# Kernel optimization log

Hardware: AMD Instinct MI355X
Metric: run time of the kernel (lower is better)

Reference implementation:

```python
import jax, jax.numpy as jnp
import numpy as np

TEMP = 0.3
EPS = 1e-09
EPS2 = 1e-10


def _unit(v):
    return v / jnp.linalg.norm(v, axis=-1, keepdims=True)


def setup_inputs() -> dict:
    key = jax.random.key(0)
    k1, k2 = jax.random.split(key)
    T, Q, D, K = 512, 8, 64, 16  # tracks, queries/track, embed dim, detections/track
    x = _unit(jax.random.normal(k1, (T * K, D), dtype=jnp.float32))
    y = _unit(jax.random.normal(k2, (T, Q, D), dtype=jnp.float32))
    track_idxs = jnp.repeat(jnp.arange(T, dtype=jnp.int64), K)  # every track id present
    return {"x": x, "track_idxs": track_idxs, "y": y}


def reference(x, track_idxs, y):
    # local_contrast=True, separate_tracks=False, static_contrast=False,
    # use_hard_condition=False, shift_to_positive=False (module defaults).
    T, Q, D = y.shape
    # All track ids 0..T-1 appear in track_idxs (by construction), so
    # ut_ids = unique(track_idxs) = arange(T) and y[ut_ids] = y.
    ut_ids = jnp.arange(T, dtype=track_idxs.dtype)
    y_flat = y.reshape(T * Q, D)          # flatten(0,1)
    y_idxs = jnp.tile(ut_ids, Q)          # ut_ids.repeat(Q) in torch semantics
    # Pairwise exp-scaled similarities: [N, T*Q]
    S = jnp.exp(jnp.einsum("nd,md->nm", x, y_flat) / TEMP)
    # Positive pairs: same track id (each x row belongs to exactly one uid),
    # so the per-uid loop collapses to one masked reduction.
    M = track_idxs[:, None] == y_idxs[None, :]
    num = jnp.sum(jnp.where(M, S, 0.0))
    den = jnp.sum(jnp.where(M, 0.0, S))
    loss = -jnp.log(num / (den + num + EPS) + EPS2)
    return loss.reshape(1)
```

## Files before the change

### kernel.cpp

```cpp
#include <hip/hip_runtime.h>
#include <hip/hip_bf16.h>

#define NROWS 8192
#define MROWS 4096
#define DDIM  64
#define TNUM  512
#define BTM   64
#define BTN   64
#define MT    4
#define GXM   (NROWS / BTM)
#define GYM   (MROWS / (BTN * MT))
#define NBLK_MAIN (GXM * GYM)
#define EXP2_SCALE 4.8089834696298780f

using bf16x8 = __attribute__((ext_vector_type(8))) short;
using f32x4  = __attribute__((ext_vector_type(4))) float;

__device__ __forceinline__ float fast_exp2(float f) {
    return __builtin_amdgcn_exp2f(f);
}
__device__ __forceinline__ short f2bf(float f) {
    __hip_bfloat16 h = __float2bfloat16(f);
    short s; __builtin_memcpy(&s, &h, 2); return s;
}

__device__ __forceinline__ int swz(int row, int colbyte) {
    return ((row << 7) + colbyte) ^ ((row & 7) << 4);
}

extern "C" __global__ __launch_bounds__(256, 4)
void ContrastiveLoss_56435870269983_kernel(
    const float* __restrict__ x, const float* __restrict__ y,
    const int* __restrict__ tid_raw,
    float2* __restrict__ part)
{
    __shared__ short ys[2][BTN * DDIM];
    __shared__ float redw[8];

    const int t    = threadIdx.x;
    const int lane = t & 63;
    const int wave = t >> 6;
    const int bid  = blockIdx.x;
    const int bx   = bid & (GXM - 1);
    const int byg  = bid >> 7;

    const int n0blk  = bx * BTM;
    const int m0base = byg * (BTN * MT);

    const int xw   = (wave >> 1) * 32;
    const int yw   = (wave & 1) * 32;
    const int rsel = lane & 15;
    const int khi  = lane >> 4;
    const int kb   = khi << 4;

    const float4* ysrc0 = (const float4*)(y + (size_t)m0base * DDIM);
    float4 sty[4];
    #pragma unroll
    for (int q = 0; q < 4; ++q) sty[q] = ysrc0[q * 256 + t];

    bf16x8 af[2][2];
    #pragma unroll
    for (int i = 0; i < 2; ++i)
        #pragma unroll
        for (int s = 0; s < 2; ++s) {
            const float* p = x + (size_t)(n0blk + xw + i * 16 + rsel) * DDIM
                               + s * 32 + khi * 8;
            float4 a0 = *(const float4*)p;
            float4 a1 = *(const float4*)(p + 4);
            bf16x8 f;
            f[0] = f2bf(a0.x * EXP2_SCALE); f[1] = f2bf(a0.y * EXP2_SCALE);
            f[2] = f2bf(a0.z * EXP2_SCALE); f[3] = f2bf(a0.w * EXP2_SCALE);
            f[4] = f2bf(a1.x * EXP2_SCALE); f[5] = f2bf(a1.y * EXP2_SCALE);
            f[6] = f2bf(a1.z * EXP2_SCALE); f[7] = f2bf(a1.w * EXP2_SCALE);
            af[i][s] = f;
        }

    const bool is64 = (tid_raw[17] != 1);
    int tia[2][4];
    bool ok = true;
    #pragma unroll
    for (int i = 0; i < 2; ++i) {
        const int base = n0blk + xw + i * 16 + khi * 4;
        if (!is64) {
            int4 v = *(const int4*)(tid_raw + base);
            tia[i][0] = v.x; tia[i][1] = v.y; tia[i][2] = v.z; tia[i][3] = v.w;
        } else {
            #pragma unroll
            for (int r = 0; r < 4; ++r) tia[i][r] = tid_raw[2 * (base + r)];
        }
        ok = ok && (tia[i][0] == tia[i][1]) && (tia[i][1] == tia[i][2])
                && (tia[i][2] == tia[i][3]);
    }
    const bool fastm = __all((int)ok);

    #pragma unroll
    for (int q = 0; q < 4; ++q) {
        const int g = q * 256 + t;
        const int row = g >> 4, c4 = g & 15;
        short4 o;
        o.x = f2bf(sty[q].x); o.y = f2bf(sty[q].y);
        o.z = f2bf(sty[q].z); o.w = f2bf(sty[q].w);
        *(short4*)((char*)ys[0] + swz(row, c4 << 3)) = o;
    }
    __syncthreads();

    float sag[4] = {0.f, 0.f, 0.f, 0.f};
    float spg[2] = {0.f, 0.f};

    #pragma unroll
    for (int mt = 0; mt < MT; ++mt) {
        float4 st[4];
        if (mt + 1 < MT) {
            const float4* ysrc =
                (const float4*)(y + (size_t)(m0base + (mt + 1) * BTN) * DDIM);
            #pragma unroll
            for (int q = 0; q < 4; ++q) st[q] = ysrc[q * 256 + t];
        }

        const short* cur = ys[mt & 1];
        f32x4 acc[2][2];
        #pragma unroll
        for (int i = 0; i < 2; ++i)
            #pragma unroll
            for (int j = 0; j < 2; ++j) acc[i][j] = (f32x4){0.f, 0.f, 0.f, 0.f};

        #pragma unroll
        for (int s = 0; s < 2; ++s) {
            bf16x8 bfr[2];
            #pragma unroll
            for (int j = 0; j < 2; ++j)
                bfr[j] = *(const bf16x8*)((const char*)cur +
                         swz(yw + j * 16 + rsel, kb + s * 64));
            #pragma unroll
            for (int i = 0; i < 2; ++i)
                #pragma unroll
                for (int j = 0; j < 2; ++j)
                    acc[i][j] = __builtin_amdgcn_mfma_f32_16x16x32_bf16(
                        af[i][s], bfr[j], acc[i][j], 0, 0, 0);
        }

        const int mrow = m0base + mt * BTN + yw;
        int yc[2];
        yc[0] = (mrow + rsel) & (TNUM - 1);
        yc[1] = (mrow + 16 + rsel) & (TNUM - 1);
        if (fastm) {
            #pragma unroll
            for (int i = 0; i < 2; ++i)
                #pragma unroll
                for (int j = 0; j < 2; ++j) {
                    float e0 = fast_exp2(acc[i][j][0]);
                    float e1 = fast_exp2(acc[i][j][1]);
                    float e2 = fast_exp2(acc[i][j][2]);
                    float e3 = fast_exp2(acc[i][j][3]);
                    float g = (e0 + e1) + (e2 + e3);
                    sag[2 * i + j] += g;
                    if (tia[i][0] == yc[j]) spg[j] += g;
                }
        } else {
            #pragma unroll
            for (int i = 0; i < 2; ++i)
                #pragma unroll
                for (int j = 0; j < 2; ++j)
                    #pragma unroll
                    for (int r = 0; r < 4; ++r) {
                        float e = fast_exp2(acc[i][j][r]);
                        sag[2 * i + j] += e;
                        if (tia[i][r] == yc[j]) spg[j] += e;
                    }
        }

        if (mt + 1 < MT) {
            short* nxt = ys[(mt + 1) & 1];
            #pragma unroll
            for (int q = 0; q < 4; ++q) {
                const int g = q * 256 + t;
                const int row = g >> 4, c4 = g & 15;
                short4 o;
                o.x = f2bf(st[q].x); o.y = f2bf(st[q].y);
                o.z = f2bf(st[q].z); o.w = f2bf(st[q].w);
                *(short4*)((char*)nxt + swz(row, c4 << 3)) = o;
            }
            __syncthreads();
        }
    }

    float sa = (sag[0] + sag[1]) + (sag[2] + sag[3]);
    float sp = spg[0] + spg[1];

    #pragma unroll
    for (int off = 32; off; off >>= 1) {
        sa += __shfl_down(sa, off, 64);
        sp += __shfl_down(sp, off, 64);
    }
    if (lane == 0) { redw[wave] = sa; redw[4 + wave] = sp; }
    __syncthreads();
    if (t == 0) {
        float A = (redw[0] + redw[1]) + (redw[2] + redw[3]);
        float P = (redw[4] + redw[5]) + (redw[6] + redw[7]);
        part[bid] = make_float2(A, P);
    }
}

extern "C" __global__ __launch_bounds__(256)
void cl_final_v17(const float2* __restrict__ part, unsigned int* __restrict__ out)
{
    __shared__ float red[2][256];
    const int t = threadIdx.x;
    float a = 0.0f, p = 0.0f;
    #pragma unroll
    for (int i = t; i < NBLK_MAIN; i += 256) {
        float2 v = part[i];
        a += v.x; p += v.y;
    }
    red[0][t] = a; red[1][t] = p;
    __syncthreads();
    for (int s = 128; s > 0; s >>= 1) {
        if (t < s) { red[0][t] += red[0][t + s]; red[1][t] += red[1][t + s]; }
        __syncthreads();
    }
    if (t == 0) {
        float total = red[0][0];
        float num   = red[1][0];
        float loss  = -__logf(num / (total + 1e-9f) + 1e-10f);
        __hip_bfloat16 bh = __float2bfloat16(loss);
        unsigned short h; __builtin_memcpy(&h, &bh, 2);
        out[0] = ((unsigned int)h << 16) | (unsigned int)h;
    }
}

extern "C" void kernel_launch(void* const* d_in, const int* in_sizes, int n_in,
                              void* d_out, int out_size, void* d_ws, size_t ws_size,
                              hipStream_t stream) {
    const float* x   = (const float*)d_in[0];
    const int*   tid = (const int*)d_in[1];
    const float* y   = (const float*)d_in[2];

    float2* part = (float2*)d_ws;
    ContrastiveLoss_56435870269983_kernel<<<NBLK_MAIN, 256, 0, stream>>>(
        x, y, tid, part);
    cl_final_v17<<<1, 256, 0, stream>>>(part, (unsigned int*)d_out);
}
```

Measured before the change: 22.31 us.

## Pre-convert inputs to bf16 in a prep kernel and drop LDS staging

Adds a prep kernel that converts x (pre-scaled) and y to bf16 in workspace, so the main kernel loads MFMA fragments straight from global memory with no LDS, no syncthreads and no per-block conversion. The grid becomes 2048 blocks, with each wave covering 32 x-rows by 128 y-columns and writing its own partial sum. A fallback fp32 path runs when the workspace is too small. The cost is an extra kernel launch and a global round trip for the bf16 copies, with y fragments re-read from L2 by many blocks.

```diff
diff --git a/kernel.cpp b/kernel.cpp
--- a/kernel.cpp
+++ b/kernel.cpp
@@ -5,12 +5,12 @@
 #define MROWS 4096
 #define DDIM  64
 #define TNUM  512
-#define BTM   64
-#define BTN   64
-#define MT    4
-#define GXM   (NROWS / BTM)
-#define GYM   (MROWS / (BTN * MT))
-#define NBLK_MAIN (GXM * GYM)
+#define XE    (NROWS * DDIM)
+#define YE    (MROWS * DDIM)
+#define GXS   256
+#define NCH   8
+#define NBLK_MAIN (GXS * NCH)
+#define NPART (NBLK_MAIN * 4)
 #define EXP2_SCALE 4.8089834696298780f
 
 using bf16x8 = __attribute__((ext_vector_type(8))) short;
@@ -24,63 +24,52 @@
     short s; __builtin_memcpy(&s, &h, 2); return s;
 }
 
-__device__ __forceinline__ int swz(int row, int colbyte) {
-    return ((row << 7) + colbyte) ^ ((row & 7) << 4);
-}
-
-extern "C" __global__ __launch_bounds__(256, 4)
+extern "C" __global__ __launch_bounds__(256)
+void cl_prep_v18(const float* __restrict__ x, const float* __restrict__ y,
+                 short* __restrict__ xb, short* __restrict__ yb)
+{
+    const int g = blockIdx.x * 256 + threadIdx.x;
+    const int NX4 = XE / 4;
+    float4 v; short* dst; float s;
+    if (g < NX4) { v = ((const float4*)x)[g];       dst = xb + 4 * (size_t)g; s = EXP2_SCALE; }
+    else         { v = ((const float4*)y)[g - NX4]; dst = yb + 4 * (size_t)(g - NX4); s = 1.0f; }
+    short4 o;
+    o.x = f2bf(v.x * s); o.y = f2bf(v.y * s);
+    o.z = f2bf(v.z * s); o.w = f2bf(v.w * s);
+    *(short4*)dst = o;
+}
+
+extern "C" __global__ __launch_bounds__(256)
 void ContrastiveLoss_56435870269983_kernel(
-    const float* __restrict__ x, const float* __restrict__ y,
-    const int* __restrict__ tid_raw,
-    float2* __restrict__ part)
+    const short* __restrict__ xb, const short* __restrict__ yb,
+    const int* __restrict__ tid_raw, float2* __restrict__ part)
 {
-    __shared__ short ys[2][BTN * DDIM];
-    __shared__ float redw[8];
-
-    const int t    = threadIdx.x;
-    const int lane = t & 63;
-    const int wave = t >> 6;
-    const int bid  = blockIdx.x;
-    const int bx   = bid & (GXM - 1);
-    const int byg  = bid >> 7;
-
-    const int n0blk  = bx * BTM;
-    const int m0base = byg * (BTN * MT);
-
-    const int xw   = (wave >> 1) * 32;
-    const int yw   = (wave & 1) * 32;
+    const int t     = threadIdx.x;
+    const int lane  = t & 63;
+    const int wave  = t >> 6;
+    const int bid   = blockIdx.x;
+    const int strip = bid & (GXS - 1);
+    const int chunk = bid >> 8;
+
+    const int n0w  = strip * 32;
+    const int m0w  = chunk * 512 + wave * 128;
     const int rsel = lane & 15;
     const int khi  = lane >> 4;
-    const int kb   = khi << 4;
-
-    const float4* ysrc0 = (const float4*)(y + (size_t)m0base * DDIM);
-    float4 sty[4];
-    #pragma unroll
-    for (int q = 0; q < 4; ++q) sty[q] = ysrc0[q * 256 + t];
 
     bf16x8 af[2][2];
     #pragma unroll
     for (int i = 0; i < 2; ++i)
         #pragma unroll
-        for (int s = 0; s < 2; ++s) {
-            const float* p = x + (size_t)(n0blk + xw + i * 16 + rsel) * DDIM
-                               + s * 32 + khi * 8;
-            float4 a0 = *(const float4*)p;
-            float4 a1 = *(const float4*)(p + 4);
-            bf16x8 f;
-            f[0] = f2bf(a0.x * EXP2_SCALE); f[1] = f2bf(a0.y * EXP2_SCALE);
-            f[2] = f2bf(a0.z * EXP2_SCALE); f[3] = f2bf(a0.w * EXP2_SCALE);
-            f[4] = f2bf(a1.x * EXP2_SCALE); f[5] = f2bf(a1.y * EXP2_SCALE);
-            f[6] = f2bf(a1.z * EXP2_SCALE); f[7] = f2bf(a1.w * EXP2_SCALE);
-            af[i][s] = f;
-        }
+        for (int s = 0; s < 2; ++s)
+            af[i][s] = *(const bf16x8*)(xb +
+                (size_t)(n0w + i * 16 + rsel) * DDIM + s * 32 + khi * 8);
 
     const bool is64 = (tid_raw[17] != 1);
     int tia[2][4];
     bool ok = true;
     #pragma unroll
     for (int i = 0; i < 2; ++i) {
-        const int base = n0blk + xw + i * 16 + khi * 4;
+        const int base = n0w + i * 16 + khi * 4;
         if (!is64) {
             int4 v = *(const int4*)(tid_raw + base);
             tia[i][0] = v.x; tia[i][1] = v.y; tia[i][2] = v.z; tia[i][3] = v.w;
@@ -93,31 +82,13 @@
     }
     const bool fastm = __all((int)ok);
 
-    #pragma unroll
-    for (int q = 0; q < 4; ++q) {
-        const int g = q * 256 + t;
-        const int row = g >> 4, c4 = g & 15;
-        short4 o;
-        o.x = f2bf(sty[q].x); o.y = f2bf(sty[q].y);
-        o.z = f2bf(sty[q].z); o.w = f2bf(sty[q].w);
-        *(short4*)((char*)ys[0] + swz(row, c4 << 3)) = o;
-    }
-    __syncthreads();
-
     float sag[4] = {0.f, 0.f, 0.f, 0.f};
     float spg[2] = {0.f, 0.f};
 
     #pragma unroll
-    for (int mt = 0; mt < MT; ++mt) {
-        float4 st[4];
-        if (mt + 1 < MT) {
-            const float4* ysrc =
-                (const float4*)(y + (size_t)(m0base + (mt + 1) * BTN) * DDIM);
-            #pragma unroll
-            for (int q = 0; q < 4; ++q) st[q] = ysrc[q * 256 + t];
-        }
-
-        const short* cur = ys[mt & 1];
+    for (int yt = 0; yt < 4; ++yt) {
+        const int m0 = m0w + yt * 32;
+
         f32x4 acc[2][2];
         #pragma unroll
         for (int i = 0; i < 2; ++i)
@@ -129,8 +100,8 @@
             bf16x8 bfr[2];
             #pragma unroll
             for (int j = 0; j < 2; ++j)
-                bfr[j] = *(const bf16x8*)((const char*)cur +
-                         swz(yw + j * 16 + rsel, kb + s * 64));
+                bfr[j] = *(const bf16x8*)(yb +
+                    (size_t)(m0 + j * 16 + rsel) * DDIM + s * 32 + khi * 8);
             #pragma unroll
             for (int i = 0; i < 2; ++i)
                 #pragma unroll
@@ -139,10 +110,9 @@
                         af[i][s], bfr[j], acc[i][j], 0, 0, 0);
         }
 
-        const int mrow = m0base + mt * BTN + yw;
         int yc[2];
-        yc[0] = (mrow + rsel) & (TNUM - 1);
-        yc[1] = (mrow + 16 + rsel) & (TNUM - 1);
+        yc[0] = (m0 + rsel) & (TNUM - 1);
+        yc[1] = (m0 + 16 + rsel) & (TNUM - 1);
         if (fastm) {
             #pragma unroll
             for (int i = 0; i < 2; ++i)
@@ -168,20 +138,6 @@
                         if (tia[i][r] == yc[j]) spg[j] += e;
                     }
         }
-
-        if (mt + 1 < MT) {
-            short* nxt = ys[(mt + 1) & 1];
-            #pragma unroll
-            for (int q = 0; q < 4; ++q) {
-                const int g = q * 256 + t;
-                const int row = g >> 4, c4 = g & 15;
-                short4 o;
-                o.x = f2bf(st[q].x); o.y = f2bf(st[q].y);
-                o.z = f2bf(st[q].z); o.w = f2bf(st[q].w);
-                *(short4*)((char*)nxt + swz(row, c4 << 3)) = o;
-            }
-            __syncthreads();
-        }
     }
 
     float sa = (sag[0] + sag[1]) + (sag[2] + sag[3]);
@@ -192,23 +148,121 @@
         sa += __shfl_down(sa, off, 64);
         sp += __shfl_down(sp, off, 64);
     }
-    if (lane == 0) { redw[wave] = sa; redw[4 + wave] = sp; }
-    __syncthreads();
-    if (t == 0) {
-        float A = (redw[0] + redw[1]) + (redw[2] + redw[3]);
-        float P = (redw[4] + redw[5]) + (redw[6] + redw[7]);
-        part[bid] = make_float2(A, P);
-    }
+    if (lane == 0) part[bid * 4 + wave] = make_float2(sa, sp);
 }
 
 extern "C" __global__ __launch_bounds__(256)
-void cl_final_v17(const float2* __restrict__ part, unsigned int* __restrict__ out)
+void cl_main_f32_v18(const float* __restrict__ x, const float* __restrict__ y,
+                     const int* __restrict__ tid_raw, float2* __restrict__ part)
+{
+    const int t     = threadIdx.x;
+    const int lane  = t & 63;
+    const int wave  = t >> 6;
+    const int bid   = blockIdx.x;
+    const int strip = bid & (GXS - 1);
+    const int chunk = bid >> 8;
+
+    const int n0w  = strip * 32;
+    const int m0w  = chunk * 512 + wave * 128;
+    const int rsel = lane & 15;
+    const int khi  = lane >> 4;
+
+    bf16x8 af[2][2];
+    #pragma unroll
+    for (int i = 0; i < 2; ++i)
+        #pragma unroll
+        for (int s = 0; s < 2; ++s) {
+            const float* p = x + (size_t)(n0w + i * 16 + rsel) * DDIM + s * 32 + khi * 8;
+            float4 a0 = *(const float4*)p;
+            float4 a1 = *(const float4*)(p + 4);
+            bf16x8 f;
+            f[0] = f2bf(a0.x * EXP2_SCALE); f[1] = f2bf(a0.y * EXP2_SCALE);
+            f[2] = f2bf(a0.z * EXP2_SCALE); f[3] = f2bf(a0.w * EXP2_SCALE);
+            f[4] = f2bf(a1.x * EXP2_SCALE); f[5] = f2bf(a1.y * EXP2_SCALE);
+            f[6] = f2bf(a1.z * EXP2_SCALE); f[7] = f2bf(a1.w * EXP2_SCALE);
+            af[i][s] = f;
+        }
+
+    const bool is64 = (tid_raw[17] != 1);
+    int tia[2][4];
+    #pragma unroll
+    for (int i = 0; i < 2; ++i) {
+        const int base = n0w + i * 16 + khi * 4;
+        if (!is64) {
+            int4 v = *(const int4*)(tid_raw + base);
+            tia[i][0] = v.x; tia[i][1] = v.y; tia[i][2] = v.z; tia[i][3] = v.w;
+        } else {
+            #pragma unroll
+            for (int r = 0; r < 4; ++r) tia[i][r] = tid_raw[2 * (base + r)];
+        }
+    }
+
+    float sag[4] = {0.f, 0.f, 0.f, 0.f};
+    float spg[2] = {0.f, 0.f};
+
+    #pragma unroll
+    for (int yt = 0; yt < 4; ++yt) {
+        const int m0 = m0w + yt * 32;
+        f32x4 acc[2][2];
+        #pragma unroll
+        for (int i = 0; i < 2; ++i)
+            #pragma unroll
+            for (int j = 0; j < 2; ++j) acc[i][j] = (f32x4){0.f, 0.f, 0.f, 0.f};
+
+        #pragma unroll
+        for (int s = 0; s < 2; ++s) {
+            bf16x8 bfr[2];
+            #pragma unroll
+            for (int j = 0; j < 2; ++j) {
+                const float* p = y + (size_t)(m0 + j * 16 + rsel) * DDIM + s * 32 + khi * 8;
+                float4 b0 = *(const float4*)p;
+                float4 b1 = *(const float4*)(p + 4);
+                bf16x8 f;
+                f[0] = f2bf(b0.x); f[1] = f2bf(b0.y); f[2] = f2bf(b0.z); f[3] = f2bf(b0.w);
+                f[4] = f2bf(b1.x); f[5] = f2bf(b1.y); f[6] = f2bf(b1.z); f[7] = f2bf(b1.w);
+                bfr[j] = f;
+            }
+            #pragma unroll
+            for (int i = 0; i < 2; ++i)
+                #pragma unroll
+                for (int j = 0; j < 2; ++j)
+                    acc[i][j] = __builtin_amdgcn_mfma_f32_16x16x32_bf16(
+                        af[i][s], bfr[j], acc[i][j], 0, 0, 0);
+        }
+
+        int yc[2];
+        yc[0] = (m0 + rsel) & (TNUM - 1);
+        yc[1] = (m0 + 16 + rsel) & (TNUM - 1);
+        #pragma unroll
+        for (int i = 0; i < 2; ++i)
+            #pragma unroll
+            for (int j = 0; j < 2; ++j)
+                #pragma unroll
+                for (int r = 0; r < 4; ++r) {
+                    float e = fast_exp2(acc[i][j][r]);
+                    sag[2 * i + j] += e;
+                    if (tia[i][r] == yc[j]) spg[j] += e;
+                }
+    }
+
+    float sa = (sag[0] + sag[1]) + (sag[2] + sag[3]);
+    float sp = spg[0] + spg[1];
+    #pragma unroll
+    for (int off = 32; off; off >>= 1) {
+        sa += __shfl_down(sa, off, 64);
+        sp += __shfl_down(sp, off, 64);
+    }
+    if (lane == 0) part[bid * 4 + wave] = make_float2(sa, sp);
+}
+
+extern "C" __global__ __launch_bounds__(256)
+void cl_final_v18(const float2* __restrict__ part, unsigned int* __restrict__ out)
 {
     __shared__ float red[2][256];
     const int t = threadIdx.x;
     float a = 0.0f, p = 0.0f;
     #pragma unroll
-    for (int i = t; i < NBLK_MAIN; i += 256) {
+    for (int i = t; i < NPART; i += 256) {
         float2 v = part[i];
         a += v.x; p += v.y;
     }
@@ -235,8 +289,18 @@
     const int*   tid = (const int*)d_in[1];
     const float* y   = (const float*)d_in[2];
 
-    float2* part = (float2*)d_ws;
-    ContrastiveLoss_56435870269983_kernel<<<NBLK_MAIN, 256, 0, stream>>>(
-        x, y, tid, part);
-    cl_final_v17<<<1, 256, 0, stream>>>(part, (unsigned int*)d_out);
-}
+    const size_t need = (size_t)(XE + YE) * 2 + (size_t)NPART * sizeof(float2);
+    if (ws_size >= need) {
+        short* xb = (short*)d_ws;
+        short* yb = xb + XE;
+        float2* part = (float2*)(yb + YE);
+        cl_prep_v18<<<(XE + YE) / 4 / 256, 256, 0, stream>>>(x, y, xb, yb);
+        ContrastiveLoss_56435870269983_kernel<<<NBLK_MAIN, 256, 0, stream>>>(
+            xb, yb, tid, part);
+        cl_final_v18<<<1, 256, 0, stream>>>(part, (unsigned int*)d_out);
+    } else {
+        float2* part = (float2*)d_ws;
+        cl_main_f32_v18<<<NBLK_MAIN, 256, 0, stream>>>(x, y, tid, part);
+        cl_final_v18<<<1, 256, 0, stream>>>(part, (unsigned int*)d_out);
+    }
+}
```

After: 40.04 us. +79.5%, slower.
